# Kernel optimization log

Hardware: AMD Instinct MI355X
Metric: run time of the kernel (lower is better)

## Reference

```python
import jax, jax.numpy as jnp
import numpy as np

NMODELS, SZ_IN, SZ_OUT, B = 128, 256, 256, 4096

def setup_inputs() -> dict:
    key = jax.random.key(0)
    k1, k2, k3, k4 = jax.random.split(key, 4)
    inp = jax.random.normal(k1, (B, SZ_IN), dtype=jnp.float32)
    agent_ids = jax.random.randint(k2, (B,), 0, NMODELS, dtype=jnp.int32)
    # Embedding tables (init ~ N(0,1) like nn.Embedding default)
    weight_lut = jax.random.normal(k3, (NMODELS, SZ_IN * SZ_OUT), dtype=jnp.float32)
    bias_lut = jax.random.normal(k4, (NMODELS, SZ_OUT), dtype=jnp.float32)
    return {"inp": inp, "agent_ids": agent_ids, "weight_lut": weight_lut, "bias_lut": bias_lut}

def reference(inp, agent_ids, weight_lut, bias_lut):
    # per-id weight gather -> [B, sz_in, sz_out]
    W = weight_lut[agent_ids].reshape(-1, SZ_IN, SZ_OUT)
    b = bias_lut[agent_ids]  # [B, sz_out]
    out = jnp.einsum('bi,bio->bo', inp, W) + b
    return out
```

## Files before the change

### kernel.cpp

```cpp
#include <hip/hip_runtime.h>

#define NMODELS 128
#define SZ_IN 256
#define SZ_OUT 256
#define MAXLIST 192
#define LDSK 264
#define NT 512
#define FRAGSTRIDE 520
#define CPB 64
#define NTILES 4
#define AROWS 64

typedef __attribute__((ext_vector_type(4))) float f32x4;
typedef __attribute__((ext_vector_type(8))) short bf16x8;
typedef __attribute__((ext_vector_type(4))) short s16x4;

__device__ __forceinline__ short f2bf(float f) {
  union { float f; unsigned u; } v;
  v.f = f;
  const unsigned r = v.u + 0x7FFFu + ((v.u >> 16) & 1u);
  return (short)(r >> 16);
}

__global__ __launch_bounds__(NT, 4) void linmulti_v13(
    const float* __restrict__ inp, const int* __restrict__ ids,
    const float* __restrict__ wlut, const float* __restrict__ blut,
    float* __restrict__ out, int B) {
  const int ch = blockIdx.x;
  const int m = blockIdx.y;
  const int tid = threadIdx.x;
  const int lane = tid & 63;
  const int wv = tid >> 6;
  const int nt = wv & 3;
  const int par = wv >> 2;
  const int q = lane >> 4;
  const int n16 = lane & 15;
  const int col = ch * CPB + nt * 16 + n16;

  __shared__ short Wfrag[32 * FRAGSTRIDE];
  __shared__ short As[AROWS * LDSK];
  __shared__ int list[MAXLIST];
  __shared__ int cnt0;

  if (tid == 0) cnt0 = 0;

  int myid[8];
#pragma unroll
  for (int v = 0; v < 8; ++v) {
    const int b = v * NT + tid;
    myid[v] = (b < B) ? ids[b] : -1;
  }

  const float* __restrict__ Wb = wlut + (size_t)m * (SZ_IN * SZ_OUT) + ch * CPB;
  f32x4 wraw[8];
#pragma unroll
  for (int v = 0; v < 8; ++v) {
    const int e4 = v * NT + tid;
    const int r = e4 >> 4;
    const int c4 = e4 & 15;
    wraw[v] = *(const f32x4*)(Wb + (size_t)r * SZ_OUT + c4 * 4);
  }

  __syncthreads();

#pragma unroll
  for (int v = 0; v < 8; ++v) {
    if (myid[v] == m) {
      const int p = atomicAdd(&cnt0, 1);
      if (p < MAXLIST) list[p] = v * NT + tid;
    }
  }
  __syncthreads();
  const int cnt = (cnt0 < MAXLIST) ? cnt0 : MAXLIST;
  if (cnt == 0) return;

  f32x4 araw[8];
#pragma unroll
  for (int v = 0; v < 8; ++v) {
    const int e4 = v * NT + tid;
    const int s = e4 >> 6;
    const int f4 = e4 & 63;
    int p = s;
    if (p > cnt - 1) p = cnt - 1;
    araw[v] = ((const f32x4*)(inp + (size_t)list[p] * SZ_IN))[f4];
  }

#pragma unroll
  for (int v = 0; v < 8; ++v) {
    const int e4 = v * NT + tid;
    const int r = e4 >> 4;
    const int c0 = (e4 & 15) * 4;
    const int kb = r >> 5;
    const int qq = (r >> 3) & 3;
    const int jj = r & 7;
#pragma unroll
    for (int e = 0; e < 4; ++e) {
      const int c = c0 + e;
      Wfrag[(kb * NTILES + (c >> 4)) * FRAGSTRIDE + ((qq * 16) + (c & 15)) * 8 + jj] =
          f2bf(wraw[v][e]);
    }
  }
  __syncthreads();

  bf16x8 bfr[8];
#pragma unroll
  for (int kb = 0; kb < 8; ++kb)
    bfr[kb] = *(const bf16x8*)(Wfrag + (kb * NTILES + nt) * FRAGSTRIDE + lane * 8);

  const float bias_c = blut[m * SZ_OUT + col];

  for (int base = 0;;) {
#pragma unroll
    for (int v = 0; v < 8; ++v) {
      const int e4 = v * NT + tid;
      const int s = e4 >> 6;
      const int f4 = e4 & 63;
      s16x4 h;
#pragma unroll
      for (int j = 0; j < 4; ++j) h[j] = f2bf(araw[v][j]);
      *(s16x4*)(As + s * LDSK + f4 * 4) = h;
    }
    __syncthreads();

    const int rows = ((cnt - base) < AROWS) ? (cnt - base) : AROWS;
    const int nchunk = (rows + 15) >> 4;
    for (int c = par; c < nchunk; c += 2) {
      f32x4 acc = (f32x4){0.f, 0.f, 0.f, 0.f};
#pragma unroll
      for (int kb = 0; kb < 8; ++kb) {
        const bf16x8 afr =
            *(const bf16x8*)(As + (c * 16 + n16) * LDSK + kb * 32 + q * 8);
        acc = __builtin_amdgcn_mfma_f32_16x16x32_bf16(afr, bfr[kb], acc, 0, 0, 0);
      }
#pragma unroll
      for (int r = 0; r < 4; ++r) {
        const int gr = base + c * 16 + q * 4 + r;
        if (gr < cnt)
          out[(size_t)list[gr] * SZ_OUT + col] = acc[r] + bias_c;
      }
    }

    base += AROWS;
    if (base >= cnt) break;
    __syncthreads();
#pragma unroll
    for (int v = 0; v < 8; ++v) {
      const int e4 = v * NT + tid;
      const int s = e4 >> 6;
      const int f4 = e4 & 63;
      int p = base + s;
      if (p > cnt - 1) p = cnt - 1;
      araw[v] = ((const f32x4*)(inp + (size_t)list[p] * SZ_IN))[f4];
    }
  }
}

extern "C" void kernel_launch(void* const* d_in, const int* in_sizes, int n_in,
                              void* d_out, int out_size, void* d_ws, size_t ws_size,
                              hipStream_t stream) {
  const float* inp = (const float*)d_in[0];
  const int* ids = (const int*)d_in[1];
  const float* wlut = (const float*)d_in[2];
  const float* blut = (const float*)d_in[3];
  float* out = (float*)d_out;
  const int B = in_sizes[1];

  linmulti_v13<<<dim3(4, NMODELS), NT, 0, stream>>>(inp, ids, wlut, blut, out, B);
}
```

Measured before the change: 84.68 us.

## Load activation MFMA fragments straight from global, drop LDS staging of A

Removes the shared-memory A tile and its barriers. Each lane now loads its own activation fragment directly from global memory, converts it with the packed bf16 conversion instruction, and feeds it into the MFMA, prefetching the first chunk before the weight staging. With less LDS in use, launch bounds are raised to allow more blocks per CU. The cost is redundant global reads of input rows across waves and column blocks, and uncoalesced per-lane loads, in exchange for fewer syncs and LDS traffic.

```diff
diff --git a/kernel.cpp b/kernel.cpp
--- a/kernel.cpp
+++ b/kernel.cpp
@@ -4,16 +4,13 @@
 #define SZ_IN 256
 #define SZ_OUT 256
 #define MAXLIST 192
-#define LDSK 264
 #define NT 512
 #define FRAGSTRIDE 520
 #define CPB 64
 #define NTILES 4
-#define AROWS 64
 
 typedef __attribute__((ext_vector_type(4))) float f32x4;
 typedef __attribute__((ext_vector_type(8))) short bf16x8;
-typedef __attribute__((ext_vector_type(4))) short s16x4;
 
 __device__ __forceinline__ short f2bf(float f) {
   union { float f; unsigned u; } v;
@@ -22,7 +19,13 @@
   return (short)(r >> 16);
 }
 
-__global__ __launch_bounds__(NT, 4) void linmulti_v13(
+__device__ __forceinline__ unsigned pkbf(float lo, float hi) {
+  unsigned r;
+  asm("v_cvt_pk_bf16_f32 %0, %1, %2" : "=v"(r) : "v"(lo), "v"(hi));
+  return r;
+}
+
+__global__ __launch_bounds__(NT, 6) void linmulti_v15(
     const float* __restrict__ inp, const int* __restrict__ ids,
     const float* __restrict__ wlut, const float* __restrict__ blut,
     float* __restrict__ out, int B) {
@@ -38,7 +41,6 @@
   const int col = ch * CPB + nt * 16 + n16;
 
   __shared__ short Wfrag[32 * FRAGSTRIDE];
-  __shared__ short As[AROWS * LDSK];
   __shared__ int list[MAXLIST];
   __shared__ int cnt0;
 
@@ -74,16 +76,13 @@
   const int cnt = (cnt0 < MAXLIST) ? cnt0 : MAXLIST;
   if (cnt == 0) return;
 
-  f32x4 araw[8];
+  int prow = par * 16 + n16;
+  if (prow > cnt - 1) prow = cnt - 1;
+  const float* __restrict__ ap0 = inp + (size_t)list[prow] * SZ_IN;
+  f32x4 apre[4];
 #pragma unroll
-  for (int v = 0; v < 8; ++v) {
-    const int e4 = v * NT + tid;
-    const int s = e4 >> 6;
-    const int f4 = e4 & 63;
-    int p = s;
-    if (p > cnt - 1) p = cnt - 1;
-    araw[v] = ((const f32x4*)(inp + (size_t)list[p] * SZ_IN))[f4];
-  }
+  for (int j = 0; j < 4; ++j)
+    apre[j] = ((const f32x4*)ap0)[(j >> 1) * 8 + q * 2 + (j & 1)];
 
 #pragma unroll
   for (int v = 0; v < 8; ++v) {
@@ -108,49 +107,41 @@
     bfr[kb] = *(const bf16x8*)(Wfrag + (kb * NTILES + nt) * FRAGSTRIDE + lane * 8);
 
   const float bias_c = blut[m * SZ_OUT + col];
+  const int nchunk = (cnt + 15) >> 4;
 
-  for (int base = 0;;) {
+  for (int c = par, first = 1; c < nchunk; c += 2, first = 0) {
+    int rr = c * 16 + n16;
+    if (rr > cnt - 1) rr = cnt - 1;
+    const float* __restrict__ ap = inp + (size_t)list[rr] * SZ_IN;
+
+    f32x4 acc = (f32x4){0.f, 0.f, 0.f, 0.f};
 #pragma unroll
-    for (int v = 0; v < 8; ++v) {
-      const int e4 = v * NT + tid;
-      const int s = e4 >> 6;
-      const int f4 = e4 & 63;
-      s16x4 h;
+    for (int h = 0; h < 4; ++h) {
+      f32x4 ar[4];
+      if (h == 0 && first) {
 #pragma unroll
-      for (int j = 0; j < 4; ++j) h[j] = f2bf(araw[v][j]);
-      *(s16x4*)(As + s * LDSK + f4 * 4) = h;
-    }
-    __syncthreads();
-
-    const int rows = ((cnt - base) < AROWS) ? (cnt - base) : AROWS;
-    const int nchunk = (rows + 15) >> 4;
-    for (int c = par; c < nchunk; c += 2) {
-      f32x4 acc = (f32x4){0.f, 0.f, 0.f, 0.f};
+        for (int j = 0; j < 4; ++j) ar[j] = apre[j];
+      } else {
 #pragma unroll
-      for (int kb = 0; kb < 8; ++kb) {
-        const bf16x8 afr =
-            *(const bf16x8*)(As + (c * 16 + n16) * LDSK + kb * 32 + q * 8);
-        acc = __builtin_amdgcn_mfma_f32_16x16x32_bf16(afr, bfr[kb], acc, 0, 0, 0);
+        for (int j = 0; j < 4; ++j)
+          ar[j] = ((const f32x4*)ap)[h * 16 + (j >> 1) * 8 + q * 2 + (j & 1)];
       }
 #pragma unroll
-      for (int r = 0; r < 4; ++r) {
-        const int gr = base + c * 16 + q * 4 + r;
-        if (gr < cnt)
-          out[(size_t)list[gr] * SZ_OUT + col] = acc[r] + bias_c;
+      for (int kk = 0; kk < 2; ++kk) {
+        union { bf16x8 v; unsigned u[4]; } afr;
+        afr.u[0] = pkbf(ar[2 * kk][0], ar[2 * kk][1]);
+        afr.u[1] = pkbf(ar[2 * kk][2], ar[2 * kk][3]);
+        afr.u[2] = pkbf(ar[2 * kk + 1][0], ar[2 * kk + 1][1]);
+        afr.u[3] = pkbf(ar[2 * kk + 1][2], ar[2 * kk + 1][3]);
+        acc = __builtin_amdgcn_mfma_f32_16x16x32_bf16(afr.v, bfr[h * 2 + kk], acc, 0, 0, 0);
       }
     }
 
-    base += AROWS;
-    if (base >= cnt) break;
-    __syncthreads();
 #pragma unroll
-    for (int v = 0; v < 8; ++v) {
-      const int e4 = v * NT + tid;
-      const int s = e4 >> 6;
-      const int f4 = e4 & 63;
-      int p = base + s;
-      if (p > cnt - 1) p = cnt - 1;
-      araw[v] = ((const f32x4*)(inp + (size_t)list[p] * SZ_IN))[f4];
+    for (int r = 0; r < 4; ++r) {
+      const int gr = c * 16 + q * 4 + r;
+      if (gr < cnt)
+        out[(size_t)list[gr] * SZ_OUT + col] = acc[r] + bias_c;
     }
   }
 }
@@ -165,5 +156,5 @@
   float* out = (float*)d_out;
   const int B = in_sizes[1];
 
-  linmulti_v13<<<dim3(4, NMODELS), NT, 0, stream>>>(inp, ids, wlut, blut, out, B);
+  linmulti_v15<<<dim3(4, NMODELS), NT, 0, stream>>>(inp, ids, wlut, blut, out, B);
 }
```

Result: slower. 89.48 us (+5.7%).
